# Performance work log

Hardware: AMD Instinct MI355X
Metric: run time of the kernel (lower is better)

Reference implementation:

```python
import jax, jax.numpy as jnp
import numpy as np

# ---- Cl(4,1) blade algebra (CGA for 3D Euclidean space) ----
_METRIC = [1.0, 1.0, 1.0, 1.0, -1.0]  # e1..e4 square +1, e5 squares -1

def _popcount(x):
    return bin(x).count('1')

def _blade_mul(a, b):
    # sign from reordering basis vectors into canonical order
    s = 0
    t = a >> 1
    while t:
        s += _popcount(t & b)
        t >>= 1
    sign = -1.0 if (s & 1) else 1.0
    shared = a & b
    for i in range(5):
        if (shared >> i) & 1:
            sign *= _METRIC[i]
    return a ^ b, sign

_EVEN = [b for b in range(32) if _popcount(b) % 2 == 0]   # 16 even blades (versor)
_ODD = [b for b in range(32) if _popcount(b) % 2 == 1]    # 16 odd blades
_G1 = [1, 2, 4, 8, 16]                                    # grade-1 blades (CGA point)
_ODD_IDX = {b: i for i, b in enumerate(_ODD)}
_G1_IDX = {b: i for i, b in enumerate(_G1)}

def _rev_sign(b):
    g = _popcount(b)
    return -1.0 if (g * (g - 1) // 2) % 2 else 1.0

# Sparse Cayley structure tensors for the sandwich product M X ~M
_T1 = np.zeros((16, 5, 16), np.float32)   # even * grade1 -> odd
for _ie, _a in enumerate(_EVEN):
    for _ip, _b in enumerate(_G1):
        _c, _s = _blade_mul(_a, _b)
        _T1[_ie, _ip, _ODD_IDX[_c]] = _s
_T2 = np.zeros((16, 16, 5), np.float32)   # odd * reverse(even) -> grade-1
for _io, _a in enumerate(_ODD):
    for _ie, _b in enumerate(_EVEN):
        _c, _s = _blade_mul(_a, _b)
        if _c in _G1_IDX:
            _T2[_io, _ie, _G1_IDX[_c]] = _s * _rev_sign(_b)
T1 = jnp.asarray(_T1)
T2 = jnp.asarray(_T2)

N_POINTS = 2097152  # 2^21 points

def setup_inputs() -> dict:
    key = jax.random.key(0)
    k1, k2 = jax.random.split(key)
    x = jax.random.normal(k1, (N_POINTS, 3), dtype=jnp.float32)
    versor = 0.1 * jax.random.normal(k2, (N_POINTS, 16), dtype=jnp.float32)
    versor = versor.at[:, 0].add(1.0)  # near-identity even versor (scalar blade is index 0)
    return {"versor": versor, "x": x}

def _cga_encode(x):
    # P = x + 0.5|x|^2 e_inf + e_0, with e_inf = e4+e5, e_0 = (e5-e4)/2
    half_sq = 0.5 * jnp.sum(x * x, axis=-1, keepdims=True)
    return jnp.concatenate([x, half_sq - 0.5, half_sq + 0.5], axis=-1)  # (..., 5)

def _sandwich(versor, point):
    mx = jnp.einsum('...e,...p,epo->...o', versor, point, T1)   # M X : odd, 16 comps
    return jnp.einsum('...o,...e,oeq->...q', mx, versor, T2)    # (M X) ~M : grade-1, 5 comps

def _cga_decode(p):
    # scale = -P . e_inf = p[e5] - p[e4]; euclidean = P_xyz / scale
    s = p[..., 4:5] - p[..., 3:4]
    return p[..., :3] / s

def reference(versor, x):
    original_dtype = x.dtype
    xf = x.astype(jnp.float32)
    vf = versor.astype(jnp.float32)
    point = _cga_encode(xf)
    transformed = _sandwich(vf, point)
    return _cga_decode(transformed).astype(original_dtype)
```

## Files before the change

kernel.cpp:

```cpp
#include <hip/hip_runtime.h>
#include <utility>


namespace cga {

__host__ __device__ constexpr int popc5(int x) {
    int c = 0;
    for (int i = 0; i < 5; ++i) c += (x >> i) & 1;
    return c;
}
__host__ __device__ constexpr int blade_of_even(int idx) {
    int cnt = 0;
    for (int b = 0; b < 32; ++b)
        if ((popc5(b) & 1) == 0) { if (cnt == idx) return b; ++cnt; }
    return 0;
}
__host__ __device__ constexpr int blade_of_odd(int idx) {
    int cnt = 0;
    for (int b = 0; b < 32; ++b)
        if ((popc5(b) & 1) == 1) { if (cnt == idx) return b; ++cnt; }
    return 0;
}
__host__ __device__ constexpr int even_index(int blade) {
    int idx = 0;
    for (int b = 0; b < blade; ++b) if ((popc5(b) & 1) == 0) ++idx;
    return idx;
}
__host__ __device__ constexpr int odd_index(int blade) {
    int idx = 0;
    for (int b = 0; b < blade; ++b) if ((popc5(b) & 1) == 1) ++idx;
    return idx;
}
__host__ __device__ constexpr int mul_sign(int a, int b) {
    int s = 0;
    for (int t = a >> 1; t; t >>= 1) s += popc5(t & b);
    int sign = (s & 1) ? -1 : 1;
    if ((a & b) & 16) sign = -sign;
    return sign;
}
__host__ __device__ constexpr int rev_sign(int b) {
    int g = popc5(b);
    return ((g * (g - 1) / 2) & 1) ? -1 : 1;
}

struct Tables {
    int t1_dst[16][5];
    int t1_sgn[16][5];
    int t2_e[16][5];
    int t2_sgn[16][5];
};

__host__ __device__ constexpr Tables make_tables() {
    Tables r{};
    for (int ie = 0; ie < 16; ++ie) {
        const int a = blade_of_even(ie);
        for (int ip = 0; ip < 5; ++ip) {
            const int b = 1 << ip;
            const int c = a ^ b;
            r.t1_dst[ie][ip] = odd_index(c);
            r.t1_sgn[ie][ip] = mul_sign(a, b);
        }
    }
    for (int io = 0; io < 16; ++io) {
        const int a = blade_of_odd(io);
        for (int iq = 0; iq < 5; ++iq) {
            const int c = 1 << iq;
            const int b = a ^ c;
            r.t2_e[io][iq]   = even_index(b);
            r.t2_sgn[io][iq] = mul_sign(a, b) * rev_sign(b);
        }
    }
    return r;
}

constexpr Tables TAB = make_tables();

}

template <int IE, int IP>
__device__ __forceinline__ void t1_term(const float (&v)[16], const float (&p)[5],
                                        float (&mx)[16]) {
    constexpr int dst = cga::TAB.t1_dst[IE][IP];
    constexpr int sgn = cga::TAB.t1_sgn[IE][IP];
    if constexpr (sgn >= 0) mx[dst] = __builtin_fmaf( v[IE], p[IP], mx[dst]);
    else                    mx[dst] = __builtin_fmaf(-v[IE], p[IP], mx[dst]);
}
template <std::size_t... I>
__device__ __forceinline__ void t1_all(const float (&v)[16], const float (&p)[5],
                                       float (&mx)[16], std::index_sequence<I...>) {
    (t1_term<(int)(I / 5), (int)(I % 5)>(v, p, mx), ...);
}
template <int IO, int IQ>
__device__ __forceinline__ void t2_term(const float (&v)[16], const float (&mx)[16],
                                        float (&q)[5]) {
    constexpr int e   = cga::TAB.t2_e[IO][IQ];
    constexpr int sgn = cga::TAB.t2_sgn[IO][IQ];
    if constexpr (sgn >= 0) q[IQ] = __builtin_fmaf( mx[IO], v[e], q[IQ]);
    else                    q[IQ] = __builtin_fmaf(-mx[IO], v[e], q[IQ]);
}
template <std::size_t... I>
__device__ __forceinline__ void t2_all(const float (&v)[16], const float (&mx)[16],
                                       float (&q)[5], std::index_sequence<I...>) {
    (t2_term<(int)(I / 5), (int)(I % 5)>(v, mx, q), ...);
}

__device__ __forceinline__ void cga_compute(const float (&v)[16],
                                            float x0, float x1, float x2,
                                            float& o0, float& o1, float& o2) {
    const float hs = 0.5f * (x0 * x0 + x1 * x1 + x2 * x2);
    const float p[5] = {x0, x1, x2, hs - 0.5f, hs + 0.5f};
    float mx[16] = {};
    t1_all(v, p, mx, std::make_index_sequence<16 * 5>{});
    float q[5] = {};
    t2_all(v, mx, q, std::make_index_sequence<16 * 5>{});
    const float inv = 1.0f / (q[4] - q[3]);
    o0 = q[0] * inv;
    o1 = q[1] * inv;
    o2 = q[2] * inv;
}

__global__ __launch_bounds__(256) void cga_tiled_kernel(
    const float* __restrict__ versor,
    const float* __restrict__ x,
    float* __restrict__ out)
{
    __shared__ float lds_v[16 * 256];
    __shared__ float lds_x[3 * 256];
    __shared__ float lds_o[3 * 256];

    const int t   = threadIdx.x;
    const int blk = blockIdx.x;

    const float4* vg = reinterpret_cast<const float4*>(versor);
    float4 f[4];
#pragma unroll
    for (int j = 0; j < 4; ++j)
        f[j] = vg[(size_t)blk * 1024 + (size_t)(j * 256 + t)];

    float4 xf = make_float4(0.f, 0.f, 0.f, 0.f);
    if (t < 192)
        xf = reinterpret_cast<const float4*>(x)[(size_t)blk * 192 + t];

    {
        const int b = t & 3;
        const int a = t >> 2;
#pragma unroll
        for (int j = 0; j < 4; ++j) {
            const int p = 64 * j + a;
            const float w4[4] = {f[j].x, f[j].y, f[j].z, f[j].w};
#pragma unroll
            for (int w = 0; w < 4; ++w) {
                const int c = 4 * b + w;
                lds_v[c * 256 + (p ^ (4 * (c & 7)))] = w4[w];
            }
        }
    }
    if (t < 192)
        reinterpret_cast<float4*>(lds_x)[t] = xf;

    __syncthreads();

    float v[16];
#pragma unroll
    for (int c = 0; c < 16; ++c)
        v[c] = lds_v[c * 256 + (t ^ (4 * (c & 7)))];

    const float x0 = lds_x[3 * t + 0];
    const float x1 = lds_x[3 * t + 1];
    const float x2 = lds_x[3 * t + 2];

    float o0, o1, o2;
    cga_compute(v, x0, x1, x2, o0, o1, o2);

    lds_o[3 * t + 0] = o0;
    lds_o[3 * t + 1] = o1;
    lds_o[3 * t + 2] = o2;

    __syncthreads();

    if (t < 192) {
        const float4 ov = reinterpret_cast<const float4*>(lds_o)[t];
        reinterpret_cast<float4*>(out)[(size_t)blk * 192 + t] = ov;
    }
}

__global__ __launch_bounds__(256) void cga_simple_kernel(
    const float* __restrict__ versor,
    const float* __restrict__ x,
    float* __restrict__ out,
    int n)
{
    const int i = blockIdx.x * blockDim.x + threadIdx.x;
    if (i >= n) return;
    const float4* v4 = reinterpret_cast<const float4*>(versor) + (size_t)i * 4;
    const float4 a0 = v4[0], a1 = v4[1], a2 = v4[2], a3 = v4[3];
    const float v[16] = {a0.x, a0.y, a0.z, a0.w, a1.x, a1.y, a1.z, a1.w,
                         a2.x, a2.y, a2.z, a2.w, a3.x, a3.y, a3.z, a3.w};
    float o0, o1, o2;
    cga_compute(v, x[(size_t)3 * i], x[(size_t)3 * i + 1], x[(size_t)3 * i + 2],
                o0, o1, o2);
    out[(size_t)3 * i + 0] = o0;
    out[(size_t)3 * i + 1] = o1;
    out[(size_t)3 * i + 2] = o2;
}

extern "C" void kernel_launch(void* const* d_in, const int* in_sizes, int n_in,
                              void* d_out, int out_size, void* d_ws, size_t ws_size,
                              hipStream_t stream) {
    const float* versor = (const float*)d_in[0];
    const float* x      = (const float*)d_in[1];
    float* out          = (float*)d_out;
    const int n = in_sizes[0] / 16;

    if ((n & 255) == 0) {
        cga_tiled_kernel<<<n / 256, 256, 0, stream>>>(versor, x, out);
    } else {
        cga_simple_kernel<<<(n + 255) / 256, 256, 0, stream>>>(versor, x, out, n);
    }
}
```

Measured before the change: 209.7 us.

## Process multiple tiles per block with register prefetch of next tile

Each block now loops over 8 tiles, issuing the global loads for the next tile into registers while the current tile is transposed through LDS and computed. This hides memory latency within a block and cuts the grid size by a factor of eight. The output staging through LDS is removed, so results are written with strided scalar stores, and raw asm barriers with lgkmcnt waits replace __syncthreads. Fewer blocks may reduce occupancy-based latency hiding, and the scalar stores may coalesce worse.

Result: slower. 216.7 us (+3.4%).

```diff
diff --git a/kernel.cpp b/kernel.cpp
--- a/kernel.cpp
+++ b/kernel.cpp
@@ -119,68 +119,79 @@
     o2 = q[2] * inv;
 }
 
-__global__ __launch_bounds__(256) void cga_tiled_kernel(
+#define CGA_BARRIER_LGKM() asm volatile("s_waitcnt lgkmcnt(0)\n\ts_barrier" ::: "memory")
+
+template <int NT>
+__global__ __launch_bounds__(256) void cga_pipe_kernel(
     const float* __restrict__ versor,
     const float* __restrict__ x,
-    float* __restrict__ out)
+    float* __restrict__ out,
+    int total_tiles)
 {
     __shared__ float lds_v[16 * 256];
     __shared__ float lds_x[3 * 256];
-    __shared__ float lds_o[3 * 256];
-
-    const int t   = threadIdx.x;
-    const int blk = blockIdx.x;
+
+    const int t = threadIdx.x;
+    int tile = blockIdx.x * NT;
+    const int tile_end = (tile + NT < total_tiles) ? (tile + NT) : total_tiles;
 
     const float4* vg = reinterpret_cast<const float4*>(versor);
+    const float4* xg = reinterpret_cast<const float4*>(x);
+
     float4 f[4];
 #pragma unroll
     for (int j = 0; j < 4; ++j)
-        f[j] = vg[(size_t)blk * 1024 + (size_t)(j * 256 + t)];
-
+        f[j] = vg[(size_t)tile * 1024 + (size_t)(j * 256 + t)];
     float4 xf = make_float4(0.f, 0.f, 0.f, 0.f);
     if (t < 192)
-        xf = reinterpret_cast<const float4*>(x)[(size_t)blk * 192 + t];
-
-    {
-        const int b = t & 3;
-        const int a = t >> 2;
-#pragma unroll
-        for (int j = 0; j < 4; ++j) {
-            const int p = 64 * j + a;
-            const float w4[4] = {f[j].x, f[j].y, f[j].z, f[j].w};
-#pragma unroll
-            for (int w = 0; w < 4; ++w) {
-                const int c = 4 * b + w;
-                lds_v[c * 256 + (p ^ (4 * (c & 7)))] = w4[w];
+        xf = xg[(size_t)tile * 192 + t];
+
+    while (tile < tile_end) {
+        {
+            const int b = t & 3;
+            const int a = t >> 2;
+#pragma unroll
+            for (int j = 0; j < 4; ++j) {
+                const int p = 64 * j + a;
+                const float w4[4] = {f[j].x, f[j].y, f[j].z, f[j].w};
+#pragma unroll
+                for (int w = 0; w < 4; ++w) {
+                    const int c = 4 * b + w;
+                    lds_v[c * 256 + (p ^ (4 * (c & 7)))] = w4[w];
+                }
             }
         }
-    }
-    if (t < 192)
-        reinterpret_cast<float4*>(lds_x)[t] = xf;
-
-    __syncthreads();
-
-    float v[16];
-#pragma unroll
-    for (int c = 0; c < 16; ++c)
-        v[c] = lds_v[c * 256 + (t ^ (4 * (c & 7)))];
-
-    const float x0 = lds_x[3 * t + 0];
-    const float x1 = lds_x[3 * t + 1];
-    const float x2 = lds_x[3 * t + 2];
-
-    float o0, o1, o2;
-    cga_compute(v, x0, x1, x2, o0, o1, o2);
-
-    lds_o[3 * t + 0] = o0;
-    lds_o[3 * t + 1] = o1;
-    lds_o[3 * t + 2] = o2;
-
-    __syncthreads();
-
-    if (t < 192) {
-        const float4 ov = reinterpret_cast<const float4*>(lds_o)[t];
-        reinterpret_cast<float4*>(out)[(size_t)blk * 192 + t] = ov;
+        if (t < 192)
+            reinterpret_cast<float4*>(lds_x)[t] = xf;
+
+        CGA_BARRIER_LGKM();
+
+        float v[16];
+#pragma unroll
+        for (int c = 0; c < 16; ++c)
+            v[c] = lds_v[c * 256 + (t ^ (4 * (c & 7)))];
+        const float x0 = lds_x[3 * t + 0];
+        const float x1 = lds_x[3 * t + 1];
+        const float x2 = lds_x[3 * t + 2];
+
+        const int cur = tile;
+        ++tile;
+        if (tile < tile_end) {
+#pragma unroll
+            for (int j = 0; j < 4; ++j)
+                f[j] = vg[(size_t)tile * 1024 + (size_t)(j * 256 + t)];
+            if (t < 192)
+                xf = xg[(size_t)tile * 192 + t];
+        }
+
+        CGA_BARRIER_LGKM();
+
+        float o0, o1, o2;
+        cga_compute(v, x0, x1, x2, o0, o1, o2);
+        const size_t base = (size_t)cur * 256 + t;
+        out[3 * base + 0] = o0;
+        out[3 * base + 1] = o1;
+        out[3 * base + 2] = o2;
     }
 }
 
@@ -213,7 +224,10 @@
     const int n = in_sizes[0] / 16;
 
     if ((n & 255) == 0) {
-        cga_tiled_kernel<<<n / 256, 256, 0, stream>>>(versor, x, out);
+        const int tiles = n / 256;
+        constexpr int NT = 8;
+        const int grid = (tiles + NT - 1) / NT;
+        cga_pipe_kernel<NT><<<grid, 256, 0, stream>>>(versor, x, out, tiles);
     } else {
         cga_simple_kernel<<<(n + 255) / 256, 256, 0, stream>>>(versor, x, out, n);
     }
```

## Replace LDS-staged tiled kernel with direct AoS loads, four points per thread

Applied to the files above, without the earlier changes.

Removes the shared-memory transpose staging and both barriers. Each thread now loads its versor directly as four float4s and its point as three scalars, for four points spaced a grid-stride apart. Issuing all loads up front gives more memory-level parallelism per thread. In exchange, global accesses are strided per lane (64-byte versor rows, 12-byte x and out) rather than fully coalesced, and register pressure rises.

Measured after the change: 212.0 us. No clear change (+1.1%).

```diff
diff --git a/kernel.cpp b/kernel.cpp
--- a/kernel.cpp
+++ b/kernel.cpp
@@ -119,68 +119,42 @@
     o2 = q[2] * inv;
 }
 
-__global__ __launch_bounds__(256) void cga_tiled_kernel(
+template <int PPT>
+__global__ __launch_bounds__(256) void cga_aos_kernel(
     const float* __restrict__ versor,
     const float* __restrict__ x,
-    float* __restrict__ out)
+    float* __restrict__ out,
+    int stride_pts)
 {
-    __shared__ float lds_v[16 * 256];
-    __shared__ float lds_x[3 * 256];
-    __shared__ float lds_o[3 * 256];
+    const int tid = blockIdx.x * blockDim.x + threadIdx.x;
 
-    const int t   = threadIdx.x;
-    const int blk = blockIdx.x;
+    float4 f[PPT][4];
+    float  xv[PPT][3];
+#pragma unroll
+    for (int k = 0; k < PPT; ++k) {
+        const size_t p = (size_t)tid + (size_t)k * stride_pts;
+        const float4* vp = reinterpret_cast<const float4*>(versor) + p * 4;
+        f[k][0] = vp[0];
+        f[k][1] = vp[1];
+        f[k][2] = vp[2];
+        f[k][3] = vp[3];
+        xv[k][0] = x[3 * p + 0];
+        xv[k][1] = x[3 * p + 1];
+        xv[k][2] = x[3 * p + 2];
+    }
 
-    const float4* vg = reinterpret_cast<const float4*>(versor);
-    float4 f[4];
 #pragma unroll
-    for (int j = 0; j < 4; ++j)
-        f[j] = vg[(size_t)blk * 1024 + (size_t)(j * 256 + t)];
-
-    float4 xf = make_float4(0.f, 0.f, 0.f, 0.f);
-    if (t < 192)
-        xf = reinterpret_cast<const float4*>(x)[(size_t)blk * 192 + t];
-
-    {
-        const int b = t & 3;
-        const int a = t >> 2;
-#pragma unroll
-        for (int j = 0; j < 4; ++j) {
-            const int p = 64 * j + a;
-            const float w4[4] = {f[j].x, f[j].y, f[j].z, f[j].w};
-#pragma unroll
-            for (int w = 0; w < 4; ++w) {
-                const int c = 4 * b + w;
-                lds_v[c * 256 + (p ^ (4 * (c & 7)))] = w4[w];
-            }
-        }
-    }
-    if (t < 192)
-        reinterpret_cast<float4*>(lds_x)[t] = xf;
-
-    __syncthreads();
-
-    float v[16];
-#pragma unroll
-    for (int c = 0; c < 16; ++c)
-        v[c] = lds_v[c * 256 + (t ^ (4 * (c & 7)))];
-
-    const float x0 = lds_x[3 * t + 0];
-    const float x1 = lds_x[3 * t + 1];
-    const float x2 = lds_x[3 * t + 2];
-
-    float o0, o1, o2;
-    cga_compute(v, x0, x1, x2, o0, o1, o2);
-
-    lds_o[3 * t + 0] = o0;
-    lds_o[3 * t + 1] = o1;
-    lds_o[3 * t + 2] = o2;
-
-    __syncthreads();
-
-    if (t < 192) {
-        const float4 ov = reinterpret_cast<const float4*>(lds_o)[t];
-        reinterpret_cast<float4*>(out)[(size_t)blk * 192 + t] = ov;
+    for (int k = 0; k < PPT; ++k) {
+        const float v[16] = {f[k][0].x, f[k][0].y, f[k][0].z, f[k][0].w,
+                             f[k][1].x, f[k][1].y, f[k][1].z, f[k][1].w,
+                             f[k][2].x, f[k][2].y, f[k][2].z, f[k][2].w,
+                             f[k][3].x, f[k][3].y, f[k][3].z, f[k][3].w};
+        float o0, o1, o2;
+        cga_compute(v, xv[k][0], xv[k][1], xv[k][2], o0, o1, o2);
+        const size_t p = (size_t)tid + (size_t)k * stride_pts;
+        out[3 * p + 0] = o0;
+        out[3 * p + 1] = o1;
+        out[3 * p + 2] = o2;
     }
 }
 
@@ -212,8 +186,11 @@
     float* out          = (float*)d_out;
     const int n = in_sizes[0] / 16;
 
-    if ((n & 255) == 0) {
-        cga_tiled_kernel<<<n / 256, 256, 0, stream>>>(versor, x, out);
+    constexpr int PPT = 4;
+    if (n % (256 * PPT) == 0) {
+        const int threads_total = n / PPT;
+        const int grid = threads_total / 256;
+        cga_aos_kernel<PPT><<<grid, 256, 0, stream>>>(versor, x, out, threads_total);
     } else {
         cga_simple_kernel<<<(n + 255) / 256, 256, 0, stream>>>(versor, x, out, n);
     }
```
